# Kernel tuning notes

Hardware: AMD Instinct MI355X
Metric: run time of the kernel (lower is better)

Reference implementation:

```python
import jax, jax.numpy as jnp
import numpy as np

N_NODES = 4096
HID = 64
N_STEP = 10
_OFFSETS = np.array([1, 2, 5, 11, 23, 47, 97, 193])  # circulant graph -> degree 16


def setup_inputs() -> dict:
    rng = np.random.default_rng(0)
    N = N_NODES
    i = np.repeat(np.arange(N), len(_OFFSETS))
    j = (i + np.tile(_OFFSETS, N)) % N
    vals = rng.normal(0.0, 0.5, i.shape).astype(np.float32)
    J = np.zeros((N, N), np.float32)
    J[i, j] = vals
    J[j, i] = vals  # symmetric coupling matrix
    row, col = np.nonzero(J)                      # E directed edges, row-major sorted
    key_fwd = row.astype(np.int64) * N + col
    rev = np.searchsorted(key_fwd, col.astype(np.int64) * N + row)  # reverse-edge index
    ru, cu = np.nonzero(np.triu(J))               # Eu upper-triangular edges
    u2e = np.searchsorted(key_fwd, ru.astype(np.int64) * N + cu)    # upper -> full edge index
    bias = rng.normal(0.0, 0.5, N).astype(np.float32)
    p = lambda *s: jnp.asarray(rng.normal(0.0, 0.1, s).astype(np.float32))
    return {
        'J': jnp.asarray(J), 'bias': jnp.asarray(bias),
        'gat_W': p(4, HID), 'gat_a': p(2 * HID, 1),
        'ci_W1': p(4, HID), 'ci_b1': jnp.zeros((HID,), jnp.float32),
        'ci_W2': p(HID, HID), 'ci_b2': jnp.zeros((HID,), jnp.float32),
        'ci_W3': p(HID, 1), 'ci_b3': jnp.zeros((1,), jnp.float32),
        'row': jnp.asarray(row.astype(np.int32)), 'col': jnp.asarray(col.astype(np.int32)),
        'rev': jnp.asarray(rev.astype(np.int32)),
        'ru': jnp.asarray(ru.astype(np.int32)), 'cu': jnp.asarray(cu.astype(np.int32)),
        'u2e': jnp.asarray(u2e.astype(np.int32)),
        'N_step': N_STEP, 'MPNNtype': 0,
    }


def reference(J, bias, gat_W, gat_a, ci_W1, ci_b1, ci_W2, ci_b2, ci_W3, ci_b3,
              row, col, rev, ru, cu, u2e, N_step, MPNNtype):
    N = J.shape[0]
    adj = (jnp.abs(J) > 0).astype(J.dtype)
    # node features: [-b, b, degree, row-sum of J]
    feat = jnp.stack([-bias, bias, adj.sum(1), J.sum(1)], axis=1)  # [N,4]
    # GAT scores: e[i,j] = leakyrelu([Wh_i || Wh_j] @ a) = leakyrelu(Wh_i@a1 + Wh_j@a2)
    Wh = feat @ gat_W                                  # [N,H]
    f1 = Wh @ gat_a[:HID, 0]
    f2 = Wh @ gat_a[HID:, 0]
    e = jax.nn.leaky_relu(f1[:, None] + f2[None, :], 0.2)
    att = jnp.where(adj > 0, jnp.exp(e), 0.0)
    Cij_matrix = 0.5 * (att + att.T)                   # [N,N]
    Cij_e = Cij_matrix[row, col]                       # [E]
    # Ci readout MLP
    h = jax.nn.relu(feat @ ci_W1 + ci_b1)
    h = jax.nn.relu(h @ ci_W2 + ci_b2)
    Ci = h @ ci_W3 + ci_b3                             # [N,1]
    dom = Ci + Cij_matrix.sum(1, keepdims=True)
    dom = jnp.sign(dom) * jnp.maximum(jnp.abs(dom), 0.1)  # clamp |.| >= 0.1
    bias_scale = bias / dom[:, 0]
    bx_scale = jnp.stack([-bias_scale, bias_scale], axis=1)  # [N,2]
    Jv = J[row, col]
    Jxy_scale = jnp.stack([jnp.stack([Jv, -Jv], -1),
                           jnp.stack([-Jv, Jv], -1)], axis=1) / Cij_e[:, None, None]  # [E,2,2]

    def node_update(em):
        # node_messages[j,:] = sum over edges (i->j) of em[e,:]
        nm = jax.ops.segment_sum(em, col, num_segments=N) / dom   # [N,2]
        lnZ = jnp.log(jnp.sum(jnp.exp(bx_scale + nm), axis=1, keepdims=True))
        return bx_scale + nm - lnZ, lnZ

    em0 = jnp.zeros((row.shape[0], 2), J.dtype)  # log of all-ones messages
    hidden0, lnZ0 = node_update(em0)

    def bp_step(carry, _):
        em, hidden, lnZ = carry
        ln_pj = hidden[row][:, :, None]     # [E,2,1]
        ln_zj = lnZ[row][:, :, None]        # [E,1,1]
        ln_mu_ij = em[rev][:, :, None]      # message on reverse edge, [E,2,1]
        M = jnp.exp(Jxy_scale + ln_pj + ln_zj - ln_mu_ij)          # [E,2,2]
        M = M / jnp.sum(jnp.max(M, axis=1), axis=1)[:, None, None]
        em_new = jnp.log(jnp.max(M ** Cij_e[:, None, None], axis=1))  # [E,2]
        hidden_new, lnZ_new = node_update(em_new)
        return (em_new, hidden_new, lnZ_new), None

    (em, hidden, lnZ), _ = jax.lax.scan(bp_step, (em0, hidden0, lnZ0), None, length=N_step)

    readout = jnp.exp(hidden)                           # [N,2]
    Js = J[ru, cu] / Cij_matrix[ru, cu]                 # [Eu]
    Jxy_u = jnp.exp(jnp.stack([jnp.stack([Js, -Js], -1),
                               jnp.stack([-Js, Js], -1)], axis=1))  # [Eu,2,2]
    temp_i = readout[cu] / jnp.exp(em[u2e])             # [Eu,2]
    temp_j = readout[ru] / jnp.exp(em[rev[u2e]])        # [Eu,2]
    pw = Jxy_u * temp_i[:, None, :] * temp_j[:, :, None]
    pw = pw / jnp.sum(pw, axis=(1, 2), keepdims=True)
    readout_pairwise = pw.reshape(-1, 4)                # [Eu,4]
    Cij_u = Cij_matrix[ru, cu]
    node_H = -jnp.sum(readout * jnp.log(readout + 1e-16), axis=1)
    edge_H = -jnp.sum(readout_pairwise * jnp.log(readout_pairwise + 1e-16), axis=1)
    node_entropy = Ci[:, 0] @ jax.lax.stop_gradient(node_H)
    edge_entropy = Cij_u @ jax.lax.stop_gradient(edge_H)
    return (readout, readout_pairwise, node_entropy + edge_entropy,
            node_entropy, edge_entropy, Ci[:, 0], Cij_u, dom)
```

## Files before the change

### kernel.cpp

```cpp
#include <hip/hip_runtime.h>
#include <cstddef>

#define TB    256
#define DEG   16
#define NSTEP 10

__global__ __launch_bounds__(TB) void k_setup1(
    const float* __restrict__ J, const float* __restrict__ bias,
    const float* __restrict__ gat_W, const float* __restrict__ gat_a,
    const float* __restrict__ W1, const float* __restrict__ b1,
    const float* __restrict__ W2, const float* __restrict__ b2,
    const float* __restrict__ W3, const float* __restrict__ b3,
    const int* __restrict__ col, int N,
    float* __restrict__ JvW, float* __restrict__ f1g, float* __restrict__ f2g,
    float* __restrict__ ci_out, float2* __restrict__ emA, float* __restrict__ ent)
{
    __shared__ float sW2[64 * 64];
    __shared__ float sh1[TB / 16][65];
    const int tidb = threadIdx.x;
    const int g = blockIdx.x * TB + tidb;
    const int i = g >> 4, t = g & 15;
    const int lane = tidb & 63;

    for (int k = tidb; k < 64 * 64; k += TB) sW2[k] = W2[k];
    if (g < 3) ent[g] = 0.0f;

    const int j = col[g];
    const float Jv = J[(size_t)i * (size_t)N + (size_t)j];
    JvW[g] = Jv;
    emA[g] = make_float2(0.0f, 0.0f);

    float rs = Jv;
    rs += __shfl_xor(rs, 1); rs += __shfl_xor(rs, 2);
    rs += __shfl_xor(rs, 4); rs += __shfl_xor(rs, 8);

    const float b = bias[i];
    const float f0 = -b, fb = b, fd = (float)DEG, fr = rs;

    float s8 = 0.0f;
    if (lane < 8) {
        int k = lane & 3;
        const float* a = gat_a + ((lane < 4) ? 0 : 64);
        for (int h = 0; h < 64; ++h) s8 += gat_W[k * 64 + h] * a[h];
    }
    const float w10 = __shfl(s8, 0), w11 = __shfl(s8, 1), w12 = __shfl(s8, 2), w13 = __shfl(s8, 3);
    const float w20 = __shfl(s8, 4), w21 = __shfl(s8, 5), w22 = __shfl(s8, 6), w23 = __shfl(s8, 7);
    const float f1i = f0 * w10 + fb * w11 + fd * w12 + fr * w13;
    const float f2i = f0 * w20 + fb * w21 + fd * w22 + fr * w23;
    if (t == 0) { f1g[i] = f1i; f2g[i] = f2i; }

    const int nib = tidb >> 4;
    __syncthreads();
    #pragma unroll
    for (int m = 0; m < 4; ++m) {
        int h = t + 16 * m;
        float a = f0 * W1[h] + fb * W1[64 + h] + fd * W1[128 + h]
                + fr * W1[192 + h] + b1[h];
        sh1[nib][h] = fmaxf(a, 0.0f);
    }
    __syncthreads();
    float civ = 0.0f;
    #pragma unroll
    for (int m = 0; m < 4; ++m) {
        int o = t + 16 * m;
        float acc = b2[o];
        for (int h = 0; h < 64; ++h) acc += sh1[nib][h] * sW2[h * 64 + o];
        civ += fmaxf(acc, 0.0f) * W3[o];
    }
    civ += __shfl_xor(civ, 1); civ += __shfl_xor(civ, 2);
    civ += __shfl_xor(civ, 4); civ += __shfl_xor(civ, 8);
    if (t == 0) ci_out[i] = civ + b3[0];
}

__global__ __launch_bounds__(TB) void k_setup2(
    const float* __restrict__ bias, const int* __restrict__ col,
    const float* __restrict__ JvW, const float* __restrict__ f1g,
    const float* __restrict__ f2g, const float* __restrict__ ci_out,
    float* __restrict__ cijW, float* __restrict__ jsW,
    float* __restrict__ domW, float* __restrict__ bsW, float* __restrict__ dom_out,
    float2* __restrict__ hidA, float* __restrict__ lnzA)
{
    const int g = blockIdx.x * TB + threadIdx.x;
    const int i = g >> 4, t = g & 15;
    const int j = col[g];
    const float Jv = JvW[g];
    const float f1i = f1g[i], f2i = f2g[i], f1j = f1g[j], f2j = f2g[j];
    float x1 = f1i + f2j; x1 = (x1 > 0.0f) ? x1 : 0.2f * x1;
    float x2 = f1j + f2i; x2 = (x2 > 0.0f) ? x2 : 0.2f * x2;
    const float C = 0.5f * (expf(x1) + expf(x2));
    cijW[g] = C; jsW[g] = Jv / C;

    float sc = C;
    sc += __shfl_xor(sc, 1); sc += __shfl_xor(sc, 2);
    sc += __shfl_xor(sc, 4); sc += __shfl_xor(sc, 8);
    const float s = ci_out[i] + sc;
    const float cl = fmaxf(fabsf(s), 0.1f);
    const float d = (s > 0.0f) ? cl : ((s < 0.0f) ? -cl : 0.0f);
    const float bs = bias[i] / d;
    if (t == 0) {
        dom_out[i] = d; domW[i] = d; bsW[i] = bs;
        float u0 = -bs, u1 = bs;
        float mm = fmaxf(u0, u1);
        float lz = mm + logf(expf(u0 - mm) + expf(u1 - mm));
        hidA[i] = make_float2(u0 - lz, u1 - lz);
        lnzA[i] = lz;
    }
}

__global__ __launch_bounds__(TB) void k_step(
    const int* __restrict__ col, const int* __restrict__ rev,
    const float* __restrict__ jsW, const float* __restrict__ cijW,
    const float* __restrict__ domW, const float* __restrict__ bsW,
    const float2* __restrict__ hidP, const float* __restrict__ lnzP,
    const float2* __restrict__ emP,
    float2* __restrict__ hidQ, float* __restrict__ lnzQ, float2* __restrict__ emQ,
    int last, const float* __restrict__ ci_out,
    float2* __restrict__ ro_out, float* __restrict__ ent)
{
    __shared__ float red[TB / 64];
    const int g = blockIdx.x * TB + threadIdx.x;
    const int i = g >> 4, t = g & 15;
    const int j = col[g], rg = rev[g];
    const float js = jsW[g], C = cijW[g];

    const float2 hj = hidP[j];
    const float lzj = lnzP[j];
    const float2 mu = emP[rg];
    const float a0 = hj.x + lzj - mu.x, a1 = hj.y + lzj - mu.y;
    const float t0 = fmaxf( js + a0, -js + a1);
    const float t1 = fmaxf(-js + a0,  js + a1);
    const float m2 = fmaxf(t0, t1);
    const float ls = m2 + logf(expf(t0 - m2) + expf(t1 - m2));
    const float e0 = C * (t0 - ls), e1 = C * (t1 - ls);
    emQ[g] = make_float2(e0, e1);

    float nm0 = e0, nm1 = e1;
    nm0 += __shfl_xor(nm0, 1); nm1 += __shfl_xor(nm1, 1);
    nm0 += __shfl_xor(nm0, 2); nm1 += __shfl_xor(nm1, 2);
    nm0 += __shfl_xor(nm0, 4); nm1 += __shfl_xor(nm1, 4);
    nm0 += __shfl_xor(nm0, 8); nm1 += __shfl_xor(nm1, 8);
    const float d = domW[i], bs = bsW[i];
    nm0 /= d; nm1 /= d;
    const float v0 = -bs + nm0, v1 = bs + nm1;
    const float mv = fmaxf(v0, v1);
    const float lzn = mv + logf(expf(v0 - mv) + expf(v1 - mv));
    const float h0 = v0 - lzn, h1 = v1 - lzn;
    if (t == 0) { hidQ[i] = make_float2(h0, h1); lnzQ[i] = lzn; }

    if (last) {
        float nodeC = 0.0f;
        if (t == 0) {
            float r0 = expf(h0), r1 = expf(h1);
            ro_out[i] = make_float2(r0, r1);
            float H = -(r0 * logf(r0 + 1e-16f) + r1 * logf(r1 + 1e-16f));
            nodeC = ci_out[i] * H;
        }
        for (int off = 32; off > 0; off >>= 1) nodeC += __shfl_down(nodeC, off);
        const int lane = threadIdx.x & 63, wv = threadIdx.x >> 6;
        if (lane == 0) red[wv] = nodeC;
        __syncthreads();
        if (threadIdx.x == 0) {
            float sn = red[0] + red[1] + red[2] + red[3];
            atomicAdd(&ent[0], sn);
            atomicAdd(&ent[1], sn);
        }
    }
}

__global__ __launch_bounds__(TB) void k_epi(
    const int* __restrict__ ru, const int* __restrict__ cu,
    const int* __restrict__ u2e, const int* __restrict__ rev,
    const float* __restrict__ jsW, const float* __restrict__ cijW,
    const float2* __restrict__ hidF, const float2* __restrict__ emF,
    float4* __restrict__ rp_out, float* __restrict__ cij_out,
    float* __restrict__ ent)
{
    __shared__ float red[TB / 64];
    const int u = blockIdx.x * TB + threadIdx.x;
    const int e = u2e[u], r = ru[u], c = cu[u];
    const int er = rev[e];
    const float jse = jsW[e];
    const float Ce  = cijW[e];
    const float2 hc = hidF[c], hr = hidF[r];
    const float2 eme = emF[er];
    const float2 emr = emF[e];
    const float ti0 = hc.x - eme.x, ti1 = hc.y - eme.y;
    const float tj0 = hr.x - emr.x, tj1 = hr.y - emr.y;
    const float L00 =  jse + ti0 + tj0;
    const float L01 = -jse + ti1 + tj0;
    const float L10 = -jse + ti0 + tj1;
    const float L11 =  jse + ti1 + tj1;
    const float mL = fmaxf(fmaxf(L00, L01), fmaxf(L10, L11));
    float p00 = expf(L00 - mL), p01 = expf(L01 - mL);
    float p10 = expf(L10 - mL), p11 = expf(L11 - mL);
    const float inv = 1.0f / (p00 + p01 + p10 + p11);
    p00 *= inv; p01 *= inv; p10 *= inv; p11 *= inv;
    rp_out[u] = make_float4(p00, p01, p10, p11);
    cij_out[u] = Ce;
    const float H = -(p00 * logf(p00 + 1e-16f) + p01 * logf(p01 + 1e-16f)
                    + p10 * logf(p10 + 1e-16f) + p11 * logf(p11 + 1e-16f));
    float edgeC = Ce * H;
    for (int off = 32; off > 0; off >>= 1) edgeC += __shfl_down(edgeC, off);
    const int lane = threadIdx.x & 63, wv = threadIdx.x >> 6;
    if (lane == 0) red[wv] = edgeC;
    __syncthreads();
    if (threadIdx.x == 0) {
        float se = red[0] + red[1] + red[2] + red[3];
        atomicAdd(&ent[0], se);
        atomicAdd(&ent[2], se);
    }
}

extern "C" void kernel_launch(void* const* d_in, const int* in_sizes, int n_in,
                              void* d_out, int out_size, void* d_ws, size_t ws_size,
                              hipStream_t stream) {
    const float* J     = (const float*)d_in[0];
    const float* bias  = (const float*)d_in[1];
    const float* gat_W = (const float*)d_in[2];
    const float* gat_a = (const float*)d_in[3];
    const float* W1    = (const float*)d_in[4];
    const float* b1    = (const float*)d_in[5];
    const float* W2    = (const float*)d_in[6];
    const float* b2    = (const float*)d_in[7];
    const float* W3    = (const float*)d_in[8];
    const float* b3    = (const float*)d_in[9];
    const int*   col   = (const int*)d_in[11];
    const int*   rev   = (const int*)d_in[12];
    const int*   ru    = (const int*)d_in[13];
    const int*   cu    = (const int*)d_in[14];
    const int*   u2e   = (const int*)d_in[15];

    const int N  = in_sizes[1];
    const int E  = in_sizes[10];
    const int Eu = in_sizes[13];

    float* out = (float*)d_out;
    size_t OFF_RP  = 2 * (size_t)N;
    size_t OFF_ENT = OFF_RP + 4 * (size_t)Eu;
    float2* ro_out  = (float2*)out;
    float4* rp_out  = (float4*)(out + OFF_RP);
    float*  ent     = out + OFF_ENT;
    float*  ci_out  = ent + 3;
    float*  cij_out = ci_out + N;
    float*  dom_out = cij_out + Eu;

    char* w = (char*)d_ws;
    auto carve = [&](size_t bytes) {
        void* q = (void*)w;
        w += (bytes + 255) & ~(size_t)255;
        return q;
    };
    float*  JvW  = (float*)carve((size_t)E * 4);
    float*  cijW = (float*)carve((size_t)E * 4);
    float*  jsW  = (float*)carve((size_t)E * 4);
    float*  f1g  = (float*)carve((size_t)N * 4);
    float*  f2g  = (float*)carve((size_t)N * 4);
    float*  domW = (float*)carve((size_t)N * 4);
    float*  bsW  = (float*)carve((size_t)N * 4);
    float2* hidA = (float2*)carve((size_t)N * 8);
    float2* hidB = (float2*)carve((size_t)N * 8);
    float*  lnzA = (float*)carve((size_t)N * 4);
    float*  lnzB = (float*)carve((size_t)N * 4);
    float2* emA  = (float2*)carve((size_t)E * 8);
    float2* emB  = (float2*)carve((size_t)E * 8);

    const int gE  = E / TB;
    const int gEu = Eu / TB;

    k_setup1<<<gE, TB, 0, stream>>>(J, bias, gat_W, gat_a, W1, b1, W2, b2, W3, b3,
                                    col, N, JvW, f1g, f2g, ci_out, emA, ent);
    k_setup2<<<gE, TB, 0, stream>>>(bias, col, JvW, f1g, f2g, ci_out,
                                    cijW, jsW, domW, bsW, dom_out, hidA, lnzA);

    float2 *hidP = hidA, *hidQ = hidB, *emP = emA, *emQ = emB;
    float  *lnzP = lnzA, *lnzQ = lnzB;
    for (int s = 0; s < NSTEP; ++s) {
        int last = (s == NSTEP - 1) ? 1 : 0;
        k_step<<<gE, TB, 0, stream>>>(col, rev, jsW, cijW, domW, bsW,
                                      hidP, lnzP, emP, hidQ, lnzQ, emQ,
                                      last, ci_out, ro_out, ent);
        float2* t2;
        t2 = hidP; hidP = hidQ; hidQ = t2;
        t2 = emP;  emP  = emQ;  emQ  = t2;
        float* t1;
        t1 = lnzP; lnzP = lnzQ; lnzQ = t1;
    }
    k_epi<<<gEu, TB, 0, stream>>>(ru, cu, u2e, rev, jsW, cijW, hidP, emP,
                                  rp_out, cij_out, ent);
}
```

Baseline: 181.4 us.

## Fuse setup kernels, pack edge data into int4, store unnormalized node beliefs

Merges the two setup kernels into one by recomputing the neighbor's J row-sum and GAT features per edge, which removes one launch and the f1/f2 round trip through global memory. Packs col, rev, js and Cij into a single int4 per edge so each BP step does one vector load instead of four scalar loads. Stores unnormalized node log-beliefs (hidden plus lnZ) as one float2, dropping the separate lnZ buffer and the per-step normalization, and skips the em read on the first step instead of zero-filling it. The fused setup kernel adds 16 redundant gathered J reads per edge.

```diff
diff --git a/kernel.cpp b/kernel.cpp
--- a/kernel.cpp
+++ b/kernel.cpp
@@ -5,15 +5,15 @@
 #define DEG   16
 #define NSTEP 10
 
-__global__ __launch_bounds__(TB) void k_setup1(
+__global__ __launch_bounds__(TB) void k_setup(
     const float* __restrict__ J, const float* __restrict__ bias,
     const float* __restrict__ gat_W, const float* __restrict__ gat_a,
     const float* __restrict__ W1, const float* __restrict__ b1,
     const float* __restrict__ W2, const float* __restrict__ b2,
     const float* __restrict__ W3, const float* __restrict__ b3,
-    const int* __restrict__ col, int N,
-    float* __restrict__ JvW, float* __restrict__ f1g, float* __restrict__ f2g,
-    float* __restrict__ ci_out, float2* __restrict__ emA, float* __restrict__ ent)
+    const int* __restrict__ col, const int* __restrict__ rev, int N,
+    int4* __restrict__ edgeP, float2* __restrict__ dbW, float2* __restrict__ uA,
+    float* __restrict__ ci_out, float* __restrict__ dom_out, float* __restrict__ ent)
 {
     __shared__ float sW2[64 * 64];
     __shared__ float sh1[TB / 16][65];
@@ -27,15 +27,20 @@
 
     const int j = col[g];
     const float Jv = J[(size_t)i * (size_t)N + (size_t)j];
-    JvW[g] = Jv;
-    emA[g] = make_float2(0.0f, 0.0f);
 
     float rs = Jv;
     rs += __shfl_xor(rs, 1); rs += __shfl_xor(rs, 2);
     rs += __shfl_xor(rs, 4); rs += __shfl_xor(rs, 8);
 
-    const float b = bias[i];
-    const float f0 = -b, fb = b, fd = (float)DEG, fr = rs;
+    float rsj = 0.0f;
+    {
+        const int* colj = col + 16 * j;
+        const float* Jrow = J + (size_t)j * (size_t)N;
+        #pragma unroll 4
+        for (int tt = 0; tt < 16; ++tt) rsj += Jrow[colj[tt]];
+    }
+
+    const float bi = bias[i], bj = bias[j];
 
     float s8 = 0.0f;
     if (lane < 8) {
@@ -45,17 +50,29 @@
     }
     const float w10 = __shfl(s8, 0), w11 = __shfl(s8, 1), w12 = __shfl(s8, 2), w13 = __shfl(s8, 3);
     const float w20 = __shfl(s8, 4), w21 = __shfl(s8, 5), w22 = __shfl(s8, 6), w23 = __shfl(s8, 7);
-    const float f1i = f0 * w10 + fb * w11 + fd * w12 + fr * w13;
-    const float f2i = f0 * w20 + fb * w21 + fd * w22 + fr * w23;
-    if (t == 0) { f1g[i] = f1i; f2g[i] = f2i; }
+    const float fd = (float)DEG;
+    const float f1i = -bi * w10 + bi * w11 + fd * w12 + rs  * w13;
+    const float f2i = -bi * w20 + bi * w21 + fd * w22 + rs  * w23;
+    const float f1j = -bj * w10 + bj * w11 + fd * w12 + rsj * w13;
+    const float f2j = -bj * w20 + bj * w21 + fd * w22 + rsj * w23;
+
+    float x1 = f1i + f2j; x1 = (x1 > 0.0f) ? x1 : 0.2f * x1;
+    float x2 = f1j + f2i; x2 = (x2 > 0.0f) ? x2 : 0.2f * x2;
+    const float C  = 0.5f * (expf(x1) + expf(x2));
+    const float js = Jv / C;
+    edgeP[g] = make_int4(j, rev[g], __float_as_int(js), __float_as_int(C));
+
+    float sc = C;
+    sc += __shfl_xor(sc, 1); sc += __shfl_xor(sc, 2);
+    sc += __shfl_xor(sc, 4); sc += __shfl_xor(sc, 8);
 
     const int nib = tidb >> 4;
     __syncthreads();
     #pragma unroll
     for (int m = 0; m < 4; ++m) {
         int h = t + 16 * m;
-        float a = f0 * W1[h] + fb * W1[64 + h] + fd * W1[128 + h]
-                + fr * W1[192 + h] + b1[h];
+        float a = -bi * W1[h] + bi * W1[64 + h] + fd * W1[128 + h]
+                + rs * W1[192 + h] + b1[h];
         sh1[nib][h] = fmaxf(a, 0.0f);
     }
     __syncthreads();
@@ -69,64 +86,37 @@
     }
     civ += __shfl_xor(civ, 1); civ += __shfl_xor(civ, 2);
     civ += __shfl_xor(civ, 4); civ += __shfl_xor(civ, 8);
-    if (t == 0) ci_out[i] = civ + b3[0];
-}
-
-__global__ __launch_bounds__(TB) void k_setup2(
-    const float* __restrict__ bias, const int* __restrict__ col,
-    const float* __restrict__ JvW, const float* __restrict__ f1g,
-    const float* __restrict__ f2g, const float* __restrict__ ci_out,
-    float* __restrict__ cijW, float* __restrict__ jsW,
-    float* __restrict__ domW, float* __restrict__ bsW, float* __restrict__ dom_out,
-    float2* __restrict__ hidA, float* __restrict__ lnzA)
-{
-    const int g = blockIdx.x * TB + threadIdx.x;
-    const int i = g >> 4, t = g & 15;
-    const int j = col[g];
-    const float Jv = JvW[g];
-    const float f1i = f1g[i], f2i = f2g[i], f1j = f1g[j], f2j = f2g[j];
-    float x1 = f1i + f2j; x1 = (x1 > 0.0f) ? x1 : 0.2f * x1;
-    float x2 = f1j + f2i; x2 = (x2 > 0.0f) ? x2 : 0.2f * x2;
-    const float C = 0.5f * (expf(x1) + expf(x2));
-    cijW[g] = C; jsW[g] = Jv / C;
-
-    float sc = C;
-    sc += __shfl_xor(sc, 1); sc += __shfl_xor(sc, 2);
-    sc += __shfl_xor(sc, 4); sc += __shfl_xor(sc, 8);
-    const float s = ci_out[i] + sc;
+    const float ci = civ + b3[0];
+
+    const float s  = ci + sc;
     const float cl = fmaxf(fabsf(s), 0.1f);
-    const float d = (s > 0.0f) ? cl : ((s < 0.0f) ? -cl : 0.0f);
-    const float bs = bias[i] / d;
+    const float d  = (s > 0.0f) ? cl : ((s < 0.0f) ? -cl : 0.0f);
+    const float bs = bi / d;
     if (t == 0) {
-        dom_out[i] = d; domW[i] = d; bsW[i] = bs;
-        float u0 = -bs, u1 = bs;
-        float mm = fmaxf(u0, u1);
-        float lz = mm + logf(expf(u0 - mm) + expf(u1 - mm));
-        hidA[i] = make_float2(u0 - lz, u1 - lz);
-        lnzA[i] = lz;
+        ci_out[i] = ci; dom_out[i] = d;
+        dbW[i] = make_float2(d, bs);
+        uA[i]  = make_float2(-bs, bs);
     }
 }
 
 __global__ __launch_bounds__(TB) void k_step(
-    const int* __restrict__ col, const int* __restrict__ rev,
-    const float* __restrict__ jsW, const float* __restrict__ cijW,
-    const float* __restrict__ domW, const float* __restrict__ bsW,
-    const float2* __restrict__ hidP, const float* __restrict__ lnzP,
-    const float2* __restrict__ emP,
-    float2* __restrict__ hidQ, float* __restrict__ lnzQ, float2* __restrict__ emQ,
-    int last, const float* __restrict__ ci_out,
+    const int4* __restrict__ edgeP, const float2* __restrict__ dbW,
+    const float2* __restrict__ uP, const float2* __restrict__ emP,
+    float2* __restrict__ uQ, float2* __restrict__ emQ,
+    int first, int last, const float* __restrict__ ci_out,
     float2* __restrict__ ro_out, float* __restrict__ ent)
 {
     __shared__ float red[TB / 64];
     const int g = blockIdx.x * TB + threadIdx.x;
     const int i = g >> 4, t = g & 15;
-    const int j = col[g], rg = rev[g];
-    const float js = jsW[g], C = cijW[g];
-
-    const float2 hj = hidP[j];
-    const float lzj = lnzP[j];
-    const float2 mu = emP[rg];
-    const float a0 = hj.x + lzj - mu.x, a1 = hj.y + lzj - mu.y;
+    const int4 ep = edgeP[g];
+    const int j = ep.x, rg = ep.y;
+    const float js = __int_as_float(ep.z), C = __int_as_float(ep.w);
+
+    const float2 uj = uP[j];
+    float mu0 = 0.0f, mu1 = 0.0f;
+    if (!first) { const float2 mu = emP[rg]; mu0 = mu.x; mu1 = mu.y; }
+    const float a0 = uj.x - mu0, a1 = uj.y - mu1;
     const float t0 = fmaxf( js + a0, -js + a1);
     const float t1 = fmaxf(-js + a0,  js + a1);
     const float m2 = fmaxf(t0, t1);
@@ -139,20 +129,18 @@
     nm0 += __shfl_xor(nm0, 2); nm1 += __shfl_xor(nm1, 2);
     nm0 += __shfl_xor(nm0, 4); nm1 += __shfl_xor(nm1, 4);
     nm0 += __shfl_xor(nm0, 8); nm1 += __shfl_xor(nm1, 8);
-    const float d = domW[i], bs = bsW[i];
-    nm0 /= d; nm1 /= d;
-    const float v0 = -bs + nm0, v1 = bs + nm1;
-    const float mv = fmaxf(v0, v1);
-    const float lzn = mv + logf(expf(v0 - mv) + expf(v1 - mv));
-    const float h0 = v0 - lzn, h1 = v1 - lzn;
-    if (t == 0) { hidQ[i] = make_float2(h0, h1); lnzQ[i] = lzn; }
+    const float2 db = dbW[i];
+    const float v0 = -db.y + nm0 / db.x, v1 = db.y + nm1 / db.x;
+    if (t == 0) uQ[i] = make_float2(v0, v1);
 
     if (last) {
         float nodeC = 0.0f;
         if (t == 0) {
-            float r0 = expf(h0), r1 = expf(h1);
+            const float mv = fmaxf(v0, v1);
+            const float lz = mv + logf(expf(v0 - mv) + expf(v1 - mv));
+            const float r0 = expf(v0 - lz), r1 = expf(v1 - lz);
             ro_out[i] = make_float2(r0, r1);
-            float H = -(r0 * logf(r0 + 1e-16f) + r1 * logf(r1 + 1e-16f));
+            const float H = -(r0 * logf(r0 + 1e-16f) + r1 * logf(r1 + 1e-16f));
             nodeC = ci_out[i] * H;
         }
         for (int off = 32; off > 0; off >>= 1) nodeC += __shfl_down(nodeC, off);
@@ -160,7 +148,7 @@
         if (lane == 0) red[wv] = nodeC;
         __syncthreads();
         if (threadIdx.x == 0) {
-            float sn = red[0] + red[1] + red[2] + red[3];
+            const float sn = red[0] + red[1] + red[2] + red[3];
             atomicAdd(&ent[0], sn);
             atomicAdd(&ent[1], sn);
         }
@@ -169,23 +157,27 @@
 
 __global__ __launch_bounds__(TB) void k_epi(
     const int* __restrict__ ru, const int* __restrict__ cu,
-    const int* __restrict__ u2e, const int* __restrict__ rev,
-    const float* __restrict__ jsW, const float* __restrict__ cijW,
-    const float2* __restrict__ hidF, const float2* __restrict__ emF,
+    const int* __restrict__ u2e, const int4* __restrict__ edgeP,
+    const float2* __restrict__ uF, const float2* __restrict__ emF,
     float4* __restrict__ rp_out, float* __restrict__ cij_out,
     float* __restrict__ ent)
 {
     __shared__ float red[TB / 64];
     const int u = blockIdx.x * TB + threadIdx.x;
     const int e = u2e[u], r = ru[u], c = cu[u];
-    const int er = rev[e];
-    const float jse = jsW[e];
-    const float Ce  = cijW[e];
-    const float2 hc = hidF[c], hr = hidF[r];
+    const int4 ep = edgeP[e];
+    const int er = ep.y;
+    const float jse = __int_as_float(ep.z), Ce = __int_as_float(ep.w);
+
+    const float2 uc = uF[c], ur = uF[r];
+    const float mc  = fmaxf(uc.x, uc.y);
+    const float lc  = mc + logf(expf(uc.x - mc) + expf(uc.y - mc));
+    const float mr  = fmaxf(ur.x, ur.y);
+    const float lr  = mr + logf(expf(ur.x - mr) + expf(ur.y - mr));
     const float2 eme = emF[er];
     const float2 emr = emF[e];
-    const float ti0 = hc.x - eme.x, ti1 = hc.y - eme.y;
-    const float tj0 = hr.x - emr.x, tj1 = hr.y - emr.y;
+    const float ti0 = (uc.x - lc) - eme.x, ti1 = (uc.y - lc) - eme.y;
+    const float tj0 = (ur.x - lr) - emr.x, tj1 = (ur.y - lr) - emr.y;
     const float L00 =  jse + ti0 + tj0;
     const float L01 = -jse + ti1 + tj0;
     const float L10 = -jse + ti0 + tj1;
@@ -205,7 +197,7 @@
     if (lane == 0) red[wv] = edgeC;
     __syncthreads();
     if (threadIdx.x == 0) {
-        float se = red[0] + red[1] + red[2] + red[3];
+        const float se = red[0] + red[1] + red[2] + red[3];
         atomicAdd(&ent[0], se);
         atomicAdd(&ent[2], se);
     }
@@ -250,41 +242,30 @@
         w += (bytes + 255) & ~(size_t)255;
         return q;
     };
-    float*  JvW  = (float*)carve((size_t)E * 4);
-    float*  cijW = (float*)carve((size_t)E * 4);
-    float*  jsW  = (float*)carve((size_t)E * 4);
-    float*  f1g  = (float*)carve((size_t)N * 4);
-    float*  f2g  = (float*)carve((size_t)N * 4);
-    float*  domW = (float*)carve((size_t)N * 4);
-    float*  bsW  = (float*)carve((size_t)N * 4);
-    float2* hidA = (float2*)carve((size_t)N * 8);
-    float2* hidB = (float2*)carve((size_t)N * 8);
-    float*  lnzA = (float*)carve((size_t)N * 4);
-    float*  lnzB = (float*)carve((size_t)N * 4);
-    float2* emA  = (float2*)carve((size_t)E * 8);
-    float2* emB  = (float2*)carve((size_t)E * 8);
+    int4*   edgeP = (int4*)carve((size_t)E * 16);
+    float2* dbW   = (float2*)carve((size_t)N * 8);
+    float2* uA    = (float2*)carve((size_t)N * 8);
+    float2* uB    = (float2*)carve((size_t)N * 8);
+    float2* emA   = (float2*)carve((size_t)E * 8);
+    float2* emB   = (float2*)carve((size_t)E * 8);
 
     const int gE  = E / TB;
     const int gEu = Eu / TB;
 
-    k_setup1<<<gE, TB, 0, stream>>>(J, bias, gat_W, gat_a, W1, b1, W2, b2, W3, b3,
-                                    col, N, JvW, f1g, f2g, ci_out, emA, ent);
-    k_setup2<<<gE, TB, 0, stream>>>(bias, col, JvW, f1g, f2g, ci_out,
-                                    cijW, jsW, domW, bsW, dom_out, hidA, lnzA);
-
-    float2 *hidP = hidA, *hidQ = hidB, *emP = emA, *emQ = emB;
-    float  *lnzP = lnzA, *lnzQ = lnzB;
+    k_setup<<<gE, TB, 0, stream>>>(J, bias, gat_W, gat_a, W1, b1, W2, b2, W3, b3,
+                                   col, rev, N, edgeP, dbW, uA,
+                                   ci_out, dom_out, ent);
+
+    float2 *uP = uA, *uQ = uB, *emP = emA, *emQ = emB;
     for (int s = 0; s < NSTEP; ++s) {
-        int last = (s == NSTEP - 1) ? 1 : 0;
-        k_step<<<gE, TB, 0, stream>>>(col, rev, jsW, cijW, domW, bsW,
-                                      hidP, lnzP, emP, hidQ, lnzQ, emQ,
-                                      last, ci_out, ro_out, ent);
-        float2* t2;
-        t2 = hidP; hidP = hidQ; hidQ = t2;
-        t2 = emP;  emP  = emQ;  emQ  = t2;
-        float* t1;
-        t1 = lnzP; lnzP = lnzQ; lnzQ = t1;
-    }
-    k_epi<<<gEu, TB, 0, stream>>>(ru, cu, u2e, rev, jsW, cijW, hidP, emP,
+        const int first = (s == 0) ? 1 : 0;
+        const int last  = (s == NSTEP - 1) ? 1 : 0;
+        k_step<<<gE, TB, 0, stream>>>(edgeP, dbW, uP, emP, uQ, emQ,
+                                      first, last, ci_out, ro_out, ent);
+        float2* tp;
+        tp = uP;  uP  = uQ;  uQ  = tp;
+        tp = emP; emP = emQ; emQ = tp;
+    }
+    k_epi<<<gEu, TB, 0, stream>>>(ru, cu, u2e, edgeP, uP, emP,
                                   rp_out, cij_out, ent);
 }
```

Result: faster. 177.2 us (-2.4%).
